# Kernel tuning notes

Measured on AMD Instinct MI355X. Metric: run time of the kernel, lower is better.

## Reference

```python
import jax, jax.numpy as jnp
import numpy as np
from jax import lax

C = 32           # cell_state_size (channels, depthwise groups)
B = 4            # batch
D = H = W = 64   # lattice dims
STEPS = 8        # propagation depth


def setup_inputs() -> dict:
    key = jax.random.key(0)
    k1, k2 = jax.random.split(key)
    cube_states = jax.random.normal(k1, (B, C, D, H, W), dtype=jnp.float32)
    # torch depthwise Conv3d weight: [C_out, C_in/groups=1, 3, 3, 3]
    weight = jax.random.normal(k2, (C, 1, 3, 3, 3), dtype=jnp.float32) * 0.1
    return {"cube_states": cube_states, "weight": weight, "depth": STEPS}


def _depthwise_conv3d(x, w):
    # x: [B, C, D, H, W], w: [C, 1, 3, 3, 3] -> depthwise via feature_group_count=C
    return lax.conv_general_dilated(
        x, w,
        window_strides=(1, 1, 1),
        padding=((1, 1), (1, 1), (1, 1)),
        dimension_numbers=("NCDHW", "OIDHW", "NCDHW"),
        feature_group_count=C,
    )


def reference(cube_states, weight, depth):
    x = cube_states
    for _ in range(depth):
        residual = _depthwise_conv3d(x, weight)
        x = jax.nn.gelu(x + residual, approximate=False)  # torch nn.GELU() is exact (erf)
    return x
```

## Files before the change

### kernel.cpp

```cpp
#include <hip/hip_runtime.h>
#include <math.h>

#define Bn 4
#define Cn 32
#define Dn 64
#define Hn 64
#define Wn 64
#define PLANE (Hn * Wn)
#define DT 16
#define LSTRIDE 68
#define LROWS 66
#define LPLANE (LROWS * LSTRIDE)

__device__ __forceinline__ float gelu_exact(float x) {
    float s = fabsf(x) * 0.70710678118654752f;
    float t = __builtin_amdgcn_rcpf(fmaf(0.3275911f, s, 1.0f));
    float P = t * fmaf(t, fmaf(t, fmaf(t, fmaf(t, 1.061405429f, -1.453152027f),
                                       1.421413741f), -0.284496736f), 0.254829592f);
    float E = __builtin_amdgcn_exp2f(-s * s * 1.4426950408889634f);
    float q = P * E;
    float hxq = 0.5f * x * q;
    return x > 0.f ? x - hxq : hxq;
}

__device__ __forceinline__ void read_row(const float* base, float f[10]) {
    float4 a = *(const float4*)(base);
    float4 b = *(const float4*)(base + 4);
    float2 c = *(const float2*)(base + 8);
    f[0] = a.x; f[1] = a.y; f[2] = a.z; f[3] = a.w;
    f[4] = b.x; f[5] = b.y; f[6] = b.z; f[7] = b.w;
    f[8] = c.x; f[9] = c.y;
}

__device__ __forceinline__ void acc_row(const float f[10], float w0t, float w1t,
                                        float w2t, float acc[8]) {
#pragma unroll
    for (int j = 0; j < 8; j++) {
        acc[j] = fmaf(f[j],     w0t, acc[j]);
        acc[j] = fmaf(f[j + 1], w1t, acc[j]);
        acc[j] = fmaf(f[j + 2], w2t, acc[j]);
    }
}

__global__ __launch_bounds__(512, 4)
void EmergentSpatialPropagation_step(const float* __restrict__ src,
                                     const float* __restrict__ wgt,
                                     float* __restrict__ dst) {
    __shared__ __align__(16) float lds[4 * LPLANE];

    const int tid = threadIdx.x;
    const int d0  = blockIdx.x * DT;
    const int c   = blockIdx.y;
    const int b   = blockIdx.z;
    const size_t base = ((size_t)(b * Cn + c)) * (size_t)(Dn * PLANE);

    for (int i = tid; i < 4 * LPLANE; i += 512) lds[i] = 0.0f;

    float wt[27];
#pragma unroll
    for (int k = 0; k < 27; k++) wt[k] = wgt[c * 27 + k];

    const int h  = (tid & 7) | ((tid >> 6) << 3);
    const int w0 = ((tid >> 3) & 7) << 3;
    const int m  = tid & 15;

    auto slot = [&](int p) -> float* { return &lds[((p + 1) & 3) * LPLANE]; };

    auto load_g = [&](int p, float4 G[2]) {
        if ((unsigned)p < (unsigned)Dn) {
            const float4* g = (const float4*)(src + base + (size_t)p * PLANE);
            G[0] = g[tid];
            G[1] = g[512 + tid];
        } else {
            G[0] = make_float4(0.f, 0.f, 0.f, 0.f);
            G[1] = make_float4(0.f, 0.f, 0.f, 0.f);
        }
    };

    auto write_plane = [&](int p, const float4 G[2]) {
        float* pl = slot(p);
#pragma unroll
        for (int i = 0; i < 2; i++) {
            int idx = i * 512 + tid;
            int row = (idx >> 4) + 1;
            float prev = __shfl_up(G[i].w, 1);
            if (m == 0) prev = 0.f;
            float4 Wv = make_float4(prev, G[i].x, G[i].y, G[i].z);
            *(float4*)(pl + row * LSTRIDE + 4 * m) = Wv;
            if (m == 15) pl[row * LSTRIDE + 64] = G[i].w;
        }
    };

    __syncthreads();
    {
        float4 Ga[2], Gb[2], Gc[2];
        load_g(d0 - 1, Ga); load_g(d0, Gb); load_g(d0 + 1, Gc);
        write_plane(d0 - 1, Ga); write_plane(d0, Gb); write_plane(d0 + 1, Gc);
    }
    __syncthreads();

    float C0[3][10], C1[3][10];
#pragma unroll
    for (int ky = 0; ky < 3; ky++)
        read_row(slot(d0) + (h + ky) * LSTRIDE + w0, C0[ky]);

    for (int it = 0; it < DT; it++) {
        const int dz = d0 + it;

        float4 G[2];
        if (it < DT - 1) load_g(dz + 2, G);

#pragma unroll
        for (int ky = 0; ky < 3; ky++)
            read_row(slot(dz + 1) + (h + ky) * LSTRIDE + w0, C1[ky]);

        float acc[8] = {0, 0, 0, 0, 0, 0, 0, 0};

#pragma unroll
        for (int ky = 0; ky < 3; ky++) {
            float T[10];
            read_row(slot(dz - 1) + (h + ky) * LSTRIDE + w0, T);
            acc_row(T, wt[ky * 3 + 0], wt[ky * 3 + 1], wt[ky * 3 + 2], acc);
        }
#pragma unroll
        for (int ky = 0; ky < 3; ky++)
            acc_row(C0[ky], wt[9 + ky * 3 + 0], wt[9 + ky * 3 + 1], wt[9 + ky * 3 + 2], acc);
#pragma unroll
        for (int ky = 0; ky < 3; ky++)
            acc_row(C1[ky], wt[18 + ky * 3 + 0], wt[18 + ky * 3 + 1], wt[18 + ky * 3 + 2], acc);

        float* dptr = dst + base + (size_t)dz * PLANE + h * Wn + w0;
        float4 o0 = make_float4(gelu_exact(C0[1][1] + acc[0]),
                                gelu_exact(C0[1][2] + acc[1]),
                                gelu_exact(C0[1][3] + acc[2]),
                                gelu_exact(C0[1][4] + acc[3]));
        float4 o1 = make_float4(gelu_exact(C0[1][5] + acc[4]),
                                gelu_exact(C0[1][6] + acc[5]),
                                gelu_exact(C0[1][7] + acc[6]),
                                gelu_exact(C0[1][8] + acc[7]));
        *(float4*)(dptr)     = o0;
        *(float4*)(dptr + 4) = o1;

        if (it < DT - 1) {
            write_plane(dz + 2, G);
            __syncthreads();
        }

#pragma unroll
        for (int ky = 0; ky < 3; ky++)
#pragma unroll
            for (int k = 0; k < 10; k++) C0[ky][k] = C1[ky][k];
    }
}

extern "C" void kernel_launch(void* const* d_in, const int* in_sizes, int n_in,
                              void* d_out, int out_size, void* d_ws, size_t ws_size,
                              hipStream_t stream) {
    const float* x   = (const float*)d_in[0];
    const float* wgt = (const float*)d_in[1];
    float* out = (float*)d_out;
    float* ws  = (float*)d_ws;

    dim3 grid(Dn / DT, Cn, Bn);
    dim3 block(512);

    const float* src = x;
    for (int s = 0; s < 8; s++) {
        float* dst = (s & 1) ? out : ws;
        EmergentSpatialPropagation_step<<<grid, block, 0, stream>>>(src, wgt, dst);
        src = dst;
    }
}
```

Before: 758.3 us.

## Split each depth tile into two H-halves with halo rows, 256-thread blocks

Each block now covers a 32-row half of the H dimension instead of the full 64-row plane. It uses 256 threads and loads the two halo rows above and below from global memory. This halves the LDS footprint per block and doubles the grid, so more blocks can be resident and more are available to spread across CUs. The cost is extra halo traffic (34 rows loaded per 32 computed) and a different thread-to-row mapping that may change LDS bank behaviour.

After: 798.8 us. 1.05x slower.

```diff
diff --git a/kernel.cpp b/kernel.cpp
--- a/kernel.cpp
+++ b/kernel.cpp
@@ -8,8 +8,9 @@
 #define Wn 64
 #define PLANE (Hn * Wn)
 #define DT 16
+#define HT 32
 #define LSTRIDE 68
-#define LROWS 66
+#define LROWS (HT + 2)
 #define LPLANE (LROWS * LSTRIDE)
 
 __device__ __forceinline__ float gelu_exact(float x) {
@@ -42,46 +43,54 @@
     }
 }
 
-__global__ __launch_bounds__(512, 4)
+__global__ __launch_bounds__(256, 4)
 void EmergentSpatialPropagation_step(const float* __restrict__ src,
                                      const float* __restrict__ wgt,
                                      float* __restrict__ dst) {
     __shared__ __align__(16) float lds[4 * LPLANE];
 
-    const int tid = threadIdx.x;
-    const int d0  = blockIdx.x * DT;
-    const int c   = blockIdx.y;
-    const int b   = blockIdx.z;
+    const int tid  = threadIdx.x;
+    const int dblk = blockIdx.x >> 1;
+    const int hblk = blockIdx.x & 1;
+    const int d0   = dblk * DT;
+    const int h0   = hblk * HT;
+    const int c    = blockIdx.y;
+    const int b    = blockIdx.z;
     const size_t base = ((size_t)(b * Cn + c)) * (size_t)(Dn * PLANE);
 
-    for (int i = tid; i < 4 * LPLANE; i += 512) lds[i] = 0.0f;
+    for (int i = tid; i < 4 * LPLANE; i += 256) lds[i] = 0.0f;
 
     float wt[27];
 #pragma unroll
     for (int k = 0; k < 27; k++) wt[k] = wgt[c * 27 + k];
 
-    const int h  = (tid & 7) | ((tid >> 6) << 3);
-    const int w0 = ((tid >> 3) & 7) << 3;
+    const int h  = tid >> 3;
+    const int w0 = (tid & 7) << 3;
     const int m  = tid & 15;
 
     auto slot = [&](int p) -> float* { return &lds[((p + 1) & 3) * LPLANE]; };
 
-    auto load_g = [&](int p, float4 G[2]) {
+    auto load_g = [&](int p, float4 G[2], float4& GH) {
+        GH = make_float4(0.f, 0.f, 0.f, 0.f);
         if ((unsigned)p < (unsigned)Dn) {
             const float4* g = (const float4*)(src + base + (size_t)p * PLANE);
-            G[0] = g[tid];
-            G[1] = g[512 + tid];
+            G[0] = g[h0 * 16 + tid];
+            G[1] = g[h0 * 16 + 256 + tid];
+            if (tid < 32) {
+                int row = (tid < 16) ? (h0 - 1) : (h0 + HT);
+                if ((unsigned)row < (unsigned)Hn) GH = g[row * 16 + (tid & 15)];
+            }
         } else {
             G[0] = make_float4(0.f, 0.f, 0.f, 0.f);
             G[1] = make_float4(0.f, 0.f, 0.f, 0.f);
         }
     };
 
-    auto write_plane = [&](int p, const float4 G[2]) {
+    auto write_plane = [&](int p, const float4 G[2], float4 GH) {
         float* pl = slot(p);
 #pragma unroll
         for (int i = 0; i < 2; i++) {
-            int idx = i * 512 + tid;
+            int idx = i * 256 + tid;
             int row = (idx >> 4) + 1;
             float prev = __shfl_up(G[i].w, 1);
             if (m == 0) prev = 0.f;
@@ -89,13 +98,21 @@
             *(float4*)(pl + row * LSTRIDE + 4 * m) = Wv;
             if (m == 15) pl[row * LSTRIDE + 64] = G[i].w;
         }
+        if (tid < 32) {
+            int prow = (tid < 16) ? 0 : (LROWS - 1);
+            float prev = __shfl_up(GH.w, 1);
+            if (m == 0) prev = 0.f;
+            float4 Wv = make_float4(prev, GH.x, GH.y, GH.z);
+            *(float4*)(pl + prow * LSTRIDE + 4 * m) = Wv;
+            if (m == 15) pl[prow * LSTRIDE + 64] = GH.w;
+        }
     };
 
     __syncthreads();
     {
-        float4 Ga[2], Gb[2], Gc[2];
-        load_g(d0 - 1, Ga); load_g(d0, Gb); load_g(d0 + 1, Gc);
-        write_plane(d0 - 1, Ga); write_plane(d0, Gb); write_plane(d0 + 1, Gc);
+        float4 Ga[2], Gb[2], Gc[2], Ha, Hb, Hc;
+        load_g(d0 - 1, Ga, Ha); load_g(d0, Gb, Hb); load_g(d0 + 1, Gc, Hc);
+        write_plane(d0 - 1, Ga, Ha); write_plane(d0, Gb, Hb); write_plane(d0 + 1, Gc, Hc);
     }
     __syncthreads();
 
@@ -107,8 +124,8 @@
     for (int it = 0; it < DT; it++) {
         const int dz = d0 + it;
 
-        float4 G[2];
-        if (it < DT - 1) load_g(dz + 2, G);
+        float4 G[2], GH;
+        if (it < DT - 1) load_g(dz + 2, G, GH);
 
 #pragma unroll
         for (int ky = 0; ky < 3; ky++)
@@ -129,7 +146,7 @@
         for (int ky = 0; ky < 3; ky++)
             acc_row(C1[ky], wt[18 + ky * 3 + 0], wt[18 + ky * 3 + 1], wt[18 + ky * 3 + 2], acc);
 
-        float* dptr = dst + base + (size_t)dz * PLANE + h * Wn + w0;
+        float* dptr = dst + base + (size_t)dz * PLANE + (h0 + h) * Wn + w0;
         float4 o0 = make_float4(gelu_exact(C0[1][1] + acc[0]),
                                 gelu_exact(C0[1][2] + acc[1]),
                                 gelu_exact(C0[1][3] + acc[2]),
@@ -142,7 +159,7 @@
         *(float4*)(dptr + 4) = o1;
 
         if (it < DT - 1) {
-            write_plane(dz + 2, G);
+            write_plane(dz + 2, G, GH);
             __syncthreads();
         }
 
@@ -161,8 +178,8 @@
     float* out = (float*)d_out;
     float* ws  = (float*)d_ws;
 
-    dim3 grid(Dn / DT, Cn, Bn);
-    dim3 block(512);
+    dim3 grid((Dn / DT) * 2, Cn, Bn);
+    dim3 block(256);
 
     const float* src = x;
     for (int s = 0; s < 8; s++) {
```
